# Optimization experiments

Hardware: AMD Instinct MI355X
Metric: run time of the kernel (lower is better)

The kernel has to match this reference:

```python
import jax, jax.numpy as jnp
import numpy as np

N = 50000
E = 800000


def sage_conv(x, edge_index, W_l, b_l, W_r):
    """PyG SAGEConv with mean aggregation.

    out = lin_l(mean_{j in N(i)} x_j) + lin_r(x_i)
    lin_l has bias, lin_r (root weight) has no bias.
    """
    src, dst = edge_index[0], edge_index[1]
    n = x.shape[0]
    msg_sum = jax.ops.segment_sum(x[src], dst, num_segments=n)          # [N, F]
    cnt = jax.ops.segment_sum(jnp.ones((edge_index.shape[1],), x.dtype), dst,
                              num_segments=n)                           # [N]
    mean = msg_sum / jnp.maximum(cnt, 1.0)[:, None]
    return mean @ W_l + b_l + x @ W_r


def setup_inputs() -> dict:
    key = jax.random.key(0)
    ks = jax.random.split(key, 10)
    dims = [(128, 128), (128, 128), (128, 64)]
    inp = {
        "x": jax.random.normal(ks[0], (N, 128), dtype=jnp.float32),
        "edge_index": jax.random.randint(ks[1], (2, E), 0, N, dtype=jnp.int64),
    }
    for i, (fi, fo) in enumerate(dims):
        scale = 1.0 / np.sqrt(fi)
        inp[f"W_l{i}"] = jax.random.uniform(ks[2 + 3 * i - (3 * i) % 1], (fi, fo), jnp.float32, -scale, scale)
        inp[f"b_l{i}"] = jnp.zeros((fo,), jnp.float32)
        inp[f"W_r{i}"] = jax.random.uniform(jax.random.fold_in(ks[3], i), (fi, fo), jnp.float32, -scale, scale)
        inp[f"W_l{i}"] = jax.random.uniform(jax.random.fold_in(ks[2], i), (fi, fo), jnp.float32, -scale, scale)
    return inp


def reference(x, edge_index, W_l0, b_l0, W_r0, W_l1, b_l1, W_r1, W_l2, b_l2, W_r2):
    # Layer 1 + relu (dropout identity in eval mode)
    h = jax.nn.relu(sage_conv(x, edge_index, W_l0, b_l0, W_r0))
    # Layer 2 + relu
    h = jax.nn.relu(sage_conv(h, edge_index, W_l1, b_l1, W_r1))
    # Output layer (no activation)
    return sage_conv(h, edge_index, W_l2, b_l2, W_r2)
```

## Files before the change

### kernel.cpp

```cpp
#include <hip/hip_runtime.h>

static inline int ceil_div(int a, int b) { return (a + b - 1) / b; }

typedef __attribute__((ext_vector_type(8))) short short8;
typedef __attribute__((ext_vector_type(4))) float f32x4;

__device__ __forceinline__ ushort bf16_rne(float v) {
  uint u = __float_as_uint(v);
  return (ushort)((u + 0x7FFFu + ((u >> 16) & 1u)) >> 16);
}


__global__ void k_zero_int(int* __restrict__ p, int n) {
  int i = blockIdx.x * blockDim.x + threadIdx.x;
  if (i < n) p[i] = 0;
}

__global__ void k_count_rank(const int* __restrict__ dst, int* __restrict__ cnt,
                             int* __restrict__ rank, int e) {
  int i0 = (blockIdx.x * blockDim.x + threadIdx.x) * 4;
  if (i0 >= e) return;
  int d[4], r[4];
  if (i0 + 3 < e) {
    int4 dv = *(const int4*)(dst + i0);
    d[0] = dv.x; d[1] = dv.y; d[2] = dv.z; d[3] = dv.w;
  } else {
#pragma unroll
    for (int j = 0; j < 4; ++j) d[j] = (i0 + j < e) ? dst[i0 + j] : 0;
  }
#pragma unroll
  for (int j = 0; j < 4; ++j)
    if (i0 + j < e) r[j] = atomicAdd(&cnt[d[j]], 1);
  if (i0 + 3 < e) {
    *(int4*)(rank + i0) = make_int4(r[0], r[1], r[2], r[3]);
  } else {
#pragma unroll
    for (int j = 0; j < 4; ++j)
      if (i0 + j < e) rank[i0 + j] = r[j];
  }
}

#define SCAN_BS 256
#define SCAN_VPT 4
#define SCAN_CHUNK (SCAN_BS * SCAN_VPT)

__global__ __launch_bounds__(SCAN_BS) void k_blocksum(const int* __restrict__ cnt,
                                                      int* __restrict__ partial, int n) {
  __shared__ int s[SCAN_BS / 64];
  const int tid = threadIdx.x;
  const int base = blockIdx.x * SCAN_CHUNK;
  int sum = 0;
#pragma unroll
  for (int j = 0; j < SCAN_VPT; ++j) {
    int i = base + tid + j * SCAN_BS;
    if (i < n) sum += cnt[i];
  }
#pragma unroll
  for (int off = 32; off > 0; off >>= 1) sum += __shfl_down(sum, off, 64);
  if ((tid & 63) == 0) s[tid >> 6] = sum;
  __syncthreads();
  if (tid == 0) {
    int t = 0;
#pragma unroll
    for (int w = 0; w < SCAN_BS / 64; ++w) t += s[w];
    partial[blockIdx.x] = t;
  }
}

__global__ __launch_bounds__(256) void k_scan_partials(int* __restrict__ partial, int p,
                                                       int* __restrict__ row_ptr, int n_nodes) {
  __shared__ int s[256];
  const int tid = threadIdx.x;
  int carry = 0;
  for (int base = 0; base < p; base += 256) {
    int i = base + tid;
    int v = (i < p) ? partial[i] : 0;
    s[tid] = v;
    __syncthreads();
    for (int off = 1; off < 256; off <<= 1) {
      int t = (tid >= off) ? s[tid - off] : 0;
      __syncthreads();
      s[tid] += t;
      __syncthreads();
    }
    if (i < p) partial[i] = carry + s[tid] - v;
    int tot = s[255];
    __syncthreads();
    carry += tot;
  }
  if (tid == 0) row_ptr[n_nodes] = carry;
}

__global__ __launch_bounds__(SCAN_BS) void k_scatter(const int* __restrict__ cnt,
                                                     const int* __restrict__ partial,
                                                     int* __restrict__ row_ptr,
                                                     float* __restrict__ inv, int n) {
  __shared__ int s[SCAN_BS];
  const int tid = threadIdx.x;
  const int base = blockIdx.x * SCAN_CHUNK;
  const int i0 = base + tid * SCAN_VPT;
  int v[SCAN_VPT];
  int cv[SCAN_VPT];
  int sum = 0;
#pragma unroll
  for (int j = 0; j < SCAN_VPT; ++j) {
    int i = i0 + j;
    int c = (i < n) ? cnt[i] : 0;
    cv[j] = c;
    v[j] = sum;
    sum += c;
  }
  s[tid] = sum;
  __syncthreads();
  for (int off = 1; off < SCAN_BS; off <<= 1) {
    int t = (tid >= off) ? s[tid - off] : 0;
    __syncthreads();
    s[tid] += t;
    __syncthreads();
  }
  const int excl = partial[blockIdx.x] + s[tid] - sum;
#pragma unroll
  for (int j = 0; j < SCAN_VPT; ++j) {
    int i = i0 + j;
    if (i < n) {
      row_ptr[i] = excl + v[j];
      inv[i] = 1.0f / (float)(cv[j] > 1 ? cv[j] : 1);
    }
  }
}

__global__ void k_place(const int* __restrict__ src, const int* __restrict__ dst,
                        const int* __restrict__ rank, const int* __restrict__ row_ptr,
                        ushort* __restrict__ csr16, int e) {
  int i0 = (blockIdx.x * blockDim.x + threadIdx.x) * 4;
  if (i0 >= e) return;
  if (i0 + 3 < e) {
    int4 dv = *(const int4*)(dst + i0);
    int4 sv = *(const int4*)(src + i0);
    int4 rv = *(const int4*)(rank + i0);
    int p0 = row_ptr[dv.x], p1 = row_ptr[dv.y], p2 = row_ptr[dv.z], p3 = row_ptr[dv.w];
    csr16[p0 + rv.x] = (ushort)sv.x;
    csr16[p1 + rv.y] = (ushort)sv.y;
    csr16[p2 + rv.z] = (ushort)sv.z;
    csr16[p3 + rv.w] = (ushort)sv.w;
  } else {
#pragma unroll
    for (int j = 0; j < 4; ++j) {
      int i = i0 + j;
      if (i < e) csr16[row_ptr[dst[i]] + rank[i]] = (ushort)src[i];
    }
  }
}

template <int FOUT>
__global__ void k_pack(const float* __restrict__ Wl, const float* __restrict__ Wr,
                       ushort* __restrict__ hi, ushort* __restrict__ lo) {
  constexpr int NCOL = 2 * FOUT;
  constexpr int NCHUNK = 4 * NCOL * 4;
  int ct = blockIdx.x * 256 + threadIdx.x;
  if (ct >= NCHUNK) return;
  const int g = ct & 3;
  const int nn = (ct >> 2) % NCOL;
  const int kt = ct / (4 * NCOL);
  uint hw[4], lw[4];
#pragma unroll
  for (int w = 0; w < 4; ++w) {
    uint h2[2], l2[2];
#pragma unroll
    for (int t = 0; t < 2; ++t) {
      int j = 2 * w + t;
      int k = kt * 32 + g * 8 + j;
      float v = (nn < FOUT) ? Wl[k * FOUT + nn] : Wr[k * FOUT + (nn - FOUT)];
      uint u = __float_as_uint(v);
      uint h = u >> 16;
      float r = v - __uint_as_float(h << 16);
      uint l = __float_as_uint(r) >> 16;
      h2[t] = h; l2[t] = l;
    }
    hw[w] = h2[0] | (h2[1] << 16);
    lw[w] = l2[0] | (l2[1] << 16);
  }
  ((uint4*)hi)[ct] = make_uint4(hw[0], hw[1], hw[2], hw[3]);
  ((uint4*)lo)[ct] = make_uint4(lw[0], lw[1], lw[2], lw[3]);
}

template <int FOUT>
__global__ __launch_bounds__(256) void k_gemm2(const float* __restrict__ hin,
                                               const ushort* __restrict__ Whi,
                                               const ushort* __restrict__ Wlo,
                                               const float* __restrict__ bias,
                                               ushort* __restrict__ Zb,
                                               float* __restrict__ R, int n) {
  constexpr int NCOL = 2 * FOUT;
  constexpr int NT = NCOL / 64;
  constexpr int MT = 2;
  __shared__ uint4 sA[2][32 * 16];

  const int tid = threadIdx.x;
  const int lane = tid & 63;
  const int wave = tid >> 6;
  const int row0 = blockIdx.x * 32;

  {
    const int srow = tid >> 3;
    const int kc = tid & 7;
    float4 f4[4];
    int g = row0 + srow;
    if (g < n) {
      const float4* hp = (const float4*)(hin + (size_t)g * 128 + kc * 16);
      f4[0] = hp[0]; f4[1] = hp[1]; f4[2] = hp[2]; f4[3] = hp[3];
    } else {
      f4[0] = f4[1] = f4[2] = f4[3] = make_float4(0.f, 0.f, 0.f, 0.f);
    }
    const float* fp = (const float*)f4;
#pragma unroll
    for (int b = 0; b < 2; ++b) {
      uint hw[4], lw[4];
#pragma unroll
      for (int w = 0; w < 4; ++w) {
        float a0 = fp[b * 8 + 2 * w], a1 = fp[b * 8 + 2 * w + 1];
        uint u0 = __float_as_uint(a0), u1 = __float_as_uint(a1);
        uint h0 = u0 >> 16, h1 = u1 >> 16;
        float r0 = a0 - __uint_as_float(h0 << 16);
        float r1 = a1 - __uint_as_float(h1 << 16);
        uint l0 = __float_as_uint(r0) >> 16, l1 = __float_as_uint(r1) >> 16;
        hw[w] = h0 | (h1 << 16);
        lw[w] = l0 | (l1 << 16);
      }
      int slot = (kc * 2 + b) ^ (srow & 7);
      sA[0][srow * 16 + slot] = make_uint4(hw[0], hw[1], hw[2], hw[3]);
      sA[1][srow * 16 + slot] = make_uint4(lw[0], lw[1], lw[2], lw[3]);
    }
  }
  __syncthreads();

  const int n0 = wave * (NCOL / 4);
  const int g16 = lane >> 4;
  const int l16 = lane & 15;

  f32x4 acc[MT][NT];
#pragma unroll
  for (int mt = 0; mt < MT; ++mt)
#pragma unroll
    for (int nt = 0; nt < NT; ++nt) acc[mt][nt] = (f32x4)(0.f);

#pragma unroll
  for (int kt = 0; kt < 4; ++kt) {
    short8 ahi[MT], alo[MT];
#pragma unroll
    for (int mt = 0; mt < MT; ++mt) {
      int row = mt * 16 + l16;
      int slot = (kt * 4 + g16) ^ (row & 7);
      ahi[mt] = *(const short8*)&sA[0][row * 16 + slot];
      alo[mt] = *(const short8*)&sA[1][row * 16 + slot];
    }
    short8 bh[NT];
#pragma unroll
    for (int nt = 0; nt < NT; ++nt) {
      size_t chunk = (size_t)(kt * NCOL + n0 + nt * 16 + l16) * 4 + g16;
      bh[nt] = *(const short8*)(Whi + chunk * 8);
    }
#pragma unroll
    for (int mt = 0; mt < MT; ++mt)
#pragma unroll
      for (int nt = 0; nt < NT; ++nt)
        acc[mt][nt] = __builtin_amdgcn_mfma_f32_16x16x32_bf16(ahi[mt], bh[nt], acc[mt][nt], 0, 0, 0);
#pragma unroll
    for (int mt = 0; mt < MT; ++mt)
#pragma unroll
      for (int nt = 0; nt < NT; ++nt)
        acc[mt][nt] = __builtin_amdgcn_mfma_f32_16x16x32_bf16(alo[mt], bh[nt], acc[mt][nt], 0, 0, 0);
    short8 bl[NT];
#pragma unroll
    for (int nt = 0; nt < NT; ++nt) {
      size_t chunk = (size_t)(kt * NCOL + n0 + nt * 16 + l16) * 4 + g16;
      bl[nt] = *(const short8*)(Wlo + chunk * 8);
    }
#pragma unroll
    for (int mt = 0; mt < MT; ++mt)
#pragma unroll
      for (int nt = 0; nt < NT; ++nt)
        acc[mt][nt] = __builtin_amdgcn_mfma_f32_16x16x32_bf16(ahi[mt], bl[nt], acc[mt][nt], 0, 0, 0);
  }

#pragma unroll
  for (int nt = 0; nt < NT; ++nt) {
    int col = n0 + nt * 16 + l16;
    bool isR = col >= FOUT;
    int cw = isR ? col - FOUT : col;
    float badd = isR ? bias[cw] : 0.f;
#pragma unroll
    for (int mt = 0; mt < MT; ++mt) {
#pragma unroll
      for (int j = 0; j < 4; ++j) {
        int row = row0 + mt * 16 + g16 * 4 + j;
        if (row < n) {
          float v = acc[mt][nt][j] + badd;
          if (isR) R[(size_t)row * FOUT + cw] = v;
          else Zb[(size_t)row * FOUT + cw] = bf16_rne(v);
        }
      }
    }
  }
}

template <int FOUT, bool RELU>
__global__ __launch_bounds__(256) void k_agg2(const ushort* __restrict__ Zb,
                                              const float* __restrict__ R,
                                              const int* __restrict__ row_ptr,
                                              const ushort* __restrict__ csr16,
                                              const float* __restrict__ inv,
                                              float* __restrict__ outp, int n) {
  constexpr int FL = FOUT / 8;
  constexpr int EG = 64 / FL;
  const int lane = threadIdx.x & 63;
  const int node = blockIdx.x * 4 + (threadIdx.x >> 6);
  if (node >= n) return;
  const int c = lane % FL;
  const int eg = lane / FL;

  const int e0 = row_ptr[node];
  const int m = row_ptr[node + 1] - e0;
  const uint4* Z4 = (const uint4*)Zb;

  float acc[8];
#pragma unroll
  for (int k = 0; k < 8; ++k) acc[k] = 0.f;

  int t = eg;
  while (t < m) {
    int ss[4];
#pragma unroll
    for (int j = 0; j < 4; ++j) {
      int tj = t + j * EG;
      int tc = (tj < m) ? tj : (m - 1);
      ss[j] = csr16[e0 + tc];
    }
    uint4 z[4];
#pragma unroll
    for (int j = 0; j < 4; ++j) z[j] = Z4[(size_t)ss[j] * FL + c];
#pragma unroll
    for (int j = 0; j < 4; ++j) {
      if (t + j * EG < m) {
        const uint* zw = (const uint*)&z[j];
#pragma unroll
        for (int w = 0; w < 4; ++w) {
          acc[2 * w]     += __uint_as_float(zw[w] << 16);
          acc[2 * w + 1] += __uint_as_float(zw[w] & 0xFFFF0000u);
        }
      }
    }
    t += 4 * EG;
  }

#pragma unroll
  for (int off = FL; off < 64; off <<= 1) {
#pragma unroll
    for (int k = 0; k < 8; ++k) acc[k] += __shfl_xor(acc[k], off, 64);
  }

  if (eg == 0) {
    const float iv = inv[node];
    const float4* Rp = (const float4*)(R + (size_t)node * FOUT + c * 8);
    float4 r0 = Rp[0], r1 = Rp[1];
    float4 o0, o1;
    o0.x = fmaf(acc[0], iv, r0.x);
    o0.y = fmaf(acc[1], iv, r0.y);
    o0.z = fmaf(acc[2], iv, r0.z);
    o0.w = fmaf(acc[3], iv, r0.w);
    o1.x = fmaf(acc[4], iv, r1.x);
    o1.y = fmaf(acc[5], iv, r1.y);
    o1.z = fmaf(acc[6], iv, r1.z);
    o1.w = fmaf(acc[7], iv, r1.w);
    if (RELU) {
      o0.x = fmaxf(o0.x, 0.f); o0.y = fmaxf(o0.y, 0.f);
      o0.z = fmaxf(o0.z, 0.f); o0.w = fmaxf(o0.w, 0.f);
      o1.x = fmaxf(o1.x, 0.f); o1.y = fmaxf(o1.y, 0.f);
      o1.z = fmaxf(o1.z, 0.f); o1.w = fmaxf(o1.w, 0.f);
    }
    float4* op = (float4*)(outp + (size_t)node * FOUT + c * 8);
    op[0] = o0;
    op[1] = o1;
  }
}


extern "C" void kernel_launch(void* const* d_in, const int* in_sizes, int n_in,
                              void* d_out, int out_size, void* d_ws, size_t ws_size,
                              hipStream_t stream) {
  const float* x   = (const float*)d_in[0];
  const int*   ei  = (const int*)d_in[1];
  const float* Wl0 = (const float*)d_in[2];
  const float* bl0 = (const float*)d_in[3];
  const float* Wr0 = (const float*)d_in[4];
  const float* Wl1 = (const float*)d_in[5];
  const float* bl1 = (const float*)d_in[6];
  const float* Wr1 = (const float*)d_in[7];
  const float* Wl2 = (const float*)d_in[8];
  const float* bl2 = (const float*)d_in[9];
  const float* Wr2 = (const float*)d_in[10];
  float* out = (float*)d_out;

  const int N = in_sizes[0] / 128;
  const int E = in_sizes[1] / 2;
  const int* src = ei;
  const int* dst = ei + E;

  char* w = (char*)d_ws;
  auto alloc = [&](size_t bytes) {
    char* p = w;
    w += (bytes + 255) & ~(size_t)255;
    return p;
  };
  int*    cnt     = (int*)alloc((size_t)N * 4);
  int*    row_ptr = (int*)alloc((size_t)(N + 1) * 4);
  int*    rank    = (int*)alloc((size_t)E * 4);
  ushort* csr16   = (ushort*)alloc((size_t)E * 2 + 256);
  float*  inv     = (float*)alloc((size_t)N * 4);
  int*    partial = (int*)alloc((size_t)ceil_div(N, SCAN_CHUNK) * 4 + 256);
  ushort* Whi0    = (ushort*)alloc((size_t)4 * 256 * 4 * 16);
  ushort* Wlo0    = (ushort*)alloc((size_t)4 * 256 * 4 * 16);
  ushort* Whi1    = (ushort*)alloc((size_t)4 * 256 * 4 * 16);
  ushort* Wlo1    = (ushort*)alloc((size_t)4 * 256 * 4 * 16);
  ushort* Whi2    = (ushort*)alloc((size_t)4 * 128 * 4 * 16);
  ushort* Wlo2    = (ushort*)alloc((size_t)4 * 128 * 4 * 16);
  ushort* BZ      = (ushort*)alloc((size_t)N * 128 * 2);
  float*  BR      = (float*)alloc((size_t)N * 128 * 4);
  float*  B0      = (float*)alloc((size_t)N * 128 * 4);
  (void)ws_size; (void)n_in; (void)out_size;

  const int P = ceil_div(N, SCAN_CHUNK);

  k_pack<128><<<16, 256, 0, stream>>>(Wl0, Wr0, Whi0, Wlo0);
  k_pack<128><<<16, 256, 0, stream>>>(Wl1, Wr1, Whi1, Wlo1);
  k_pack<64><<<8, 256, 0, stream>>>(Wl2, Wr2, Whi2, Wlo2);

  k_zero_int<<<ceil_div(N, 256), 256, 0, stream>>>(cnt, N);
  k_count_rank<<<ceil_div(E, 1024), 256, 0, stream>>>(dst, cnt, rank, E);
  k_blocksum<<<P, SCAN_BS, 0, stream>>>(cnt, partial, N);
  k_scan_partials<<<1, 256, 0, stream>>>(partial, P, row_ptr, N);
  k_scatter<<<P, SCAN_BS, 0, stream>>>(cnt, partial, row_ptr, inv, N);
  k_place<<<ceil_div(E, 1024), 256, 0, stream>>>(src, dst, rank, row_ptr, csr16, E);

  k_gemm2<128><<<ceil_div(N, 32), 256, 0, stream>>>(x, Whi0, Wlo0, bl0, BZ, BR, N);
  k_agg2<128, true><<<ceil_div(N, 4), 256, 0, stream>>>(BZ, BR, row_ptr, csr16, inv, B0, N);

  k_gemm2<128><<<ceil_div(N, 32), 256, 0, stream>>>(B0, Whi1, Wlo1, bl1, BZ, BR, N);
  k_agg2<128, true><<<ceil_div(N, 4), 256, 0, stream>>>(BZ, BR, row_ptr, csr16, inv, B0, N);

  k_gemm2<64><<<ceil_div(N, 32), 256, 0, stream>>>(B0, Whi2, Wlo2, bl2, BZ, BR, N);
  k_agg2<64, false><<<ceil_div(N, 4), 256, 0, stream>>>(BZ, BR, row_ptr, csr16, inv, out, N);
}
```

Measured before the change: 236.9 us.

## Switch GEMMs to single-pass bf16 inputs and store intermediate activations as bf16

Replaces the split hi/lo bf16 emulation of fp32 GEMM (three MFMA passes) with a single bf16 pass, rounding weights and activations to bf16. Inter-layer activations are written by the aggregation kernel as bf16 instead of fp32, and a new conversion kernel casts x to bf16 up front. Edge rank storage shrinks from int to ushort. This cuts MFMA work and activation memory traffic, but loses precision relative to fp32, which may exceed tolerance, and the ushort rank assumes per-node degree below 65536.

```diff
diff --git a/kernel.cpp b/kernel.cpp
--- a/kernel.cpp
+++ b/kernel.cpp
@@ -16,8 +16,21 @@
   if (i < n) p[i] = 0;
 }
 
+__global__ void k_cvt(const float* __restrict__ in, ushort* __restrict__ outp, int n8) {
+  int i = blockIdx.x * blockDim.x + threadIdx.x;
+  if (i >= n8) return;
+  const float4* ip = (const float4*)(in + (size_t)i * 8);
+  float4 a = ip[0], b = ip[1];
+  uint p0 = (uint)bf16_rne(a.x) | ((uint)bf16_rne(a.y) << 16);
+  uint p1 = (uint)bf16_rne(a.z) | ((uint)bf16_rne(a.w) << 16);
+  uint p2 = (uint)bf16_rne(b.x) | ((uint)bf16_rne(b.y) << 16);
+  uint p3 = (uint)bf16_rne(b.z) | ((uint)bf16_rne(b.w) << 16);
+  ((uint4*)outp)[i] = make_uint4(p0, p1, p2, p3);
+}
+
+
 __global__ void k_count_rank(const int* __restrict__ dst, int* __restrict__ cnt,
-                             int* __restrict__ rank, int e) {
+                             ushort* __restrict__ rank, int e) {
   int i0 = (blockIdx.x * blockDim.x + threadIdx.x) * 4;
   if (i0 >= e) return;
   int d[4], r[4];
@@ -32,11 +45,14 @@
   for (int j = 0; j < 4; ++j)
     if (i0 + j < e) r[j] = atomicAdd(&cnt[d[j]], 1);
   if (i0 + 3 < e) {
-    *(int4*)(rank + i0) = make_int4(r[0], r[1], r[2], r[3]);
+    ushort4 rv;
+    rv.x = (ushort)r[0]; rv.y = (ushort)r[1];
+    rv.z = (ushort)r[2]; rv.w = (ushort)r[3];
+    *(ushort4*)(rank + i0) = rv;
   } else {
 #pragma unroll
     for (int j = 0; j < 4; ++j)
-      if (i0 + j < e) rank[i0 + j] = r[j];
+      if (i0 + j < e) rank[i0 + j] = (ushort)r[j];
   }
 }
 
@@ -130,14 +146,14 @@
 }
 
 __global__ void k_place(const int* __restrict__ src, const int* __restrict__ dst,
-                        const int* __restrict__ rank, const int* __restrict__ row_ptr,
+                        const ushort* __restrict__ rank, const int* __restrict__ row_ptr,
                         ushort* __restrict__ csr16, int e) {
   int i0 = (blockIdx.x * blockDim.x + threadIdx.x) * 4;
   if (i0 >= e) return;
   if (i0 + 3 < e) {
     int4 dv = *(const int4*)(dst + i0);
     int4 sv = *(const int4*)(src + i0);
-    int4 rv = *(const int4*)(rank + i0);
+    ushort4 rv = *(const ushort4*)(rank + i0);
     int p0 = row_ptr[dv.x], p1 = row_ptr[dv.y], p2 = row_ptr[dv.z], p3 = row_ptr[dv.w];
     csr16[p0 + rv.x] = (ushort)sv.x;
     csr16[p1 + rv.y] = (ushort)sv.y;
@@ -154,7 +170,7 @@
 
 template <int FOUT>
 __global__ void k_pack(const float* __restrict__ Wl, const float* __restrict__ Wr,
-                       ushort* __restrict__ hi, ushort* __restrict__ lo) {
+                       ushort* __restrict__ hi) {
   constexpr int NCOL = 2 * FOUT;
   constexpr int NCHUNK = 4 * NCOL * 4;
   int ct = blockIdx.x * 256 + threadIdx.x;
@@ -162,75 +178,45 @@
   const int g = ct & 3;
   const int nn = (ct >> 2) % NCOL;
   const int kt = ct / (4 * NCOL);
-  uint hw[4], lw[4];
+  uint hw[4];
 #pragma unroll
   for (int w = 0; w < 4; ++w) {
-    uint h2[2], l2[2];
+    uint h2[2];
 #pragma unroll
     for (int t = 0; t < 2; ++t) {
       int j = 2 * w + t;
       int k = kt * 32 + g * 8 + j;
       float v = (nn < FOUT) ? Wl[k * FOUT + nn] : Wr[k * FOUT + (nn - FOUT)];
-      uint u = __float_as_uint(v);
-      uint h = u >> 16;
-      float r = v - __uint_as_float(h << 16);
-      uint l = __float_as_uint(r) >> 16;
-      h2[t] = h; l2[t] = l;
+      h2[t] = (uint)bf16_rne(v);
     }
     hw[w] = h2[0] | (h2[1] << 16);
-    lw[w] = l2[0] | (l2[1] << 16);
   }
   ((uint4*)hi)[ct] = make_uint4(hw[0], hw[1], hw[2], hw[3]);
-  ((uint4*)lo)[ct] = make_uint4(lw[0], lw[1], lw[2], lw[3]);
 }
 
 template <int FOUT>
-__global__ __launch_bounds__(256) void k_gemm2(const float* __restrict__ hin,
-                                               const ushort* __restrict__ Whi,
-                                               const ushort* __restrict__ Wlo,
-                                               const float* __restrict__ bias,
-                                               ushort* __restrict__ Zb,
-                                               float* __restrict__ R, int n) {
+__global__ __launch_bounds__(256) void k_gemm2b(const ushort* __restrict__ Hb,
+                                                const ushort* __restrict__ Whi,
+                                                const float* __restrict__ bias,
+                                                ushort* __restrict__ Zb,
+                                                float* __restrict__ R, int n) {
   constexpr int NCOL = 2 * FOUT;
   constexpr int NT = NCOL / 64;
   constexpr int MT = 2;
-  __shared__ uint4 sA[2][32 * 16];
+  __shared__ uint4 sA[32 * 16];
 
   const int tid = threadIdx.x;
   const int lane = tid & 63;
   const int wave = tid >> 6;
   const int row0 = blockIdx.x * 32;
 
-  {
-    const int srow = tid >> 3;
-    const int kc = tid & 7;
-    float4 f4[4];
+#pragma unroll
+  for (int c = tid; c < 512; c += 256) {
+    int srow = c >> 4, col16 = c & 15;
     int g = row0 + srow;
-    if (g < n) {
-      const float4* hp = (const float4*)(hin + (size_t)g * 128 + kc * 16);
-      f4[0] = hp[0]; f4[1] = hp[1]; f4[2] = hp[2]; f4[3] = hp[3];
-    } else {
-      f4[0] = f4[1] = f4[2] = f4[3] = make_float4(0.f, 0.f, 0.f, 0.f);
-    }
-    const float* fp = (const float*)f4;
-#pragma unroll
-    for (int b = 0; b < 2; ++b) {
-      uint hw[4], lw[4];
-#pragma unroll
-      for (int w = 0; w < 4; ++w) {
-        float a0 = fp[b * 8 + 2 * w], a1 = fp[b * 8 + 2 * w + 1];
-        uint u0 = __float_as_uint(a0), u1 = __float_as_uint(a1);
-        uint h0 = u0 >> 16, h1 = u1 >> 16;
-        float r0 = a0 - __uint_as_float(h0 << 16);
-        float r1 = a1 - __uint_as_float(h1 << 16);
-        uint l0 = __float_as_uint(r0) >> 16, l1 = __float_as_uint(r1) >> 16;
-        hw[w] = h0 | (h1 << 16);
-        lw[w] = l0 | (l1 << 16);
-      }
-      int slot = (kc * 2 + b) ^ (srow & 7);
-      sA[0][srow * 16 + slot] = make_uint4(hw[0], hw[1], hw[2], hw[3]);
-      sA[1][srow * 16 + slot] = make_uint4(lw[0], lw[1], lw[2], lw[3]);
-    }
+    uint4 v = make_uint4(0u, 0u, 0u, 0u);
+    if (g < n) v = *(const uint4*)(Hb + (size_t)g * 128 + col16 * 8);
+    sA[srow * 16 + (col16 ^ (srow & 7))] = v;
   }
   __syncthreads();
 
@@ -246,13 +232,12 @@
 
 #pragma unroll
   for (int kt = 0; kt < 4; ++kt) {
-    short8 ahi[MT], alo[MT];
+    short8 a[MT];
 #pragma unroll
     for (int mt = 0; mt < MT; ++mt) {
       int row = mt * 16 + l16;
       int slot = (kt * 4 + g16) ^ (row & 7);
-      ahi[mt] = *(const short8*)&sA[0][row * 16 + slot];
-      alo[mt] = *(const short8*)&sA[1][row * 16 + slot];
+      a[mt] = *(const short8*)&sA[row * 16 + slot];
     }
     short8 bh[NT];
 #pragma unroll
@@ -264,23 +249,7 @@
     for (int mt = 0; mt < MT; ++mt)
 #pragma unroll
       for (int nt = 0; nt < NT; ++nt)
-        acc[mt][nt] = __builtin_amdgcn_mfma_f32_16x16x32_bf16(ahi[mt], bh[nt], acc[mt][nt], 0, 0, 0);
-#pragma unroll
-    for (int mt = 0; mt < MT; ++mt)
-#pragma unroll
-      for (int nt = 0; nt < NT; ++nt)
-        acc[mt][nt] = __builtin_amdgcn_mfma_f32_16x16x32_bf16(alo[mt], bh[nt], acc[mt][nt], 0, 0, 0);
-    short8 bl[NT];
-#pragma unroll
-    for (int nt = 0; nt < NT; ++nt) {
-      size_t chunk = (size_t)(kt * NCOL + n0 + nt * 16 + l16) * 4 + g16;
-      bl[nt] = *(const short8*)(Wlo + chunk * 8);
-    }
-#pragma unroll
-    for (int mt = 0; mt < MT; ++mt)
-#pragma unroll
-      for (int nt = 0; nt < NT; ++nt)
-        acc[mt][nt] = __builtin_amdgcn_mfma_f32_16x16x32_bf16(ahi[mt], bl[nt], acc[mt][nt], 0, 0, 0);
+        acc[mt][nt] = __builtin_amdgcn_mfma_f32_16x16x32_bf16(a[mt], bh[nt], acc[mt][nt], 0, 0, 0);
   }
 
 #pragma unroll
@@ -304,13 +273,13 @@
   }
 }
 
-template <int FOUT, bool RELU>
+template <int FOUT, bool RELU, bool OUTB>
 __global__ __launch_bounds__(256) void k_agg2(const ushort* __restrict__ Zb,
                                               const float* __restrict__ R,
                                               const int* __restrict__ row_ptr,
                                               const ushort* __restrict__ csr16,
                                               const float* __restrict__ inv,
-                                              float* __restrict__ outp, int n) {
+                                              void* __restrict__ outp, int n) {
   constexpr int FL = FOUT / 8;
   constexpr int EG = 64 / FL;
   const int lane = threadIdx.x & 63;
@@ -363,24 +332,30 @@
     const float iv = inv[node];
     const float4* Rp = (const float4*)(R + (size_t)node * FOUT + c * 8);
     float4 r0 = Rp[0], r1 = Rp[1];
-    float4 o0, o1;
-    o0.x = fmaf(acc[0], iv, r0.x);
-    o0.y = fmaf(acc[1], iv, r0.y);
-    o0.z = fmaf(acc[2], iv, r0.z);
-    o0.w = fmaf(acc[3], iv, r0.w);
-    o1.x = fmaf(acc[4], iv, r1.x);
-    o1.y = fmaf(acc[5], iv, r1.y);
-    o1.z = fmaf(acc[6], iv, r1.z);
-    o1.w = fmaf(acc[7], iv, r1.w);
+    float o[8];
+    o[0] = fmaf(acc[0], iv, r0.x);
+    o[1] = fmaf(acc[1], iv, r0.y);
+    o[2] = fmaf(acc[2], iv, r0.z);
+    o[3] = fmaf(acc[3], iv, r0.w);
+    o[4] = fmaf(acc[4], iv, r1.x);
+    o[5] = fmaf(acc[5], iv, r1.y);
+    o[6] = fmaf(acc[6], iv, r1.z);
+    o[7] = fmaf(acc[7], iv, r1.w);
     if (RELU) {
-      o0.x = fmaxf(o0.x, 0.f); o0.y = fmaxf(o0.y, 0.f);
-      o0.z = fmaxf(o0.z, 0.f); o0.w = fmaxf(o0.w, 0.f);
-      o1.x = fmaxf(o1.x, 0.f); o1.y = fmaxf(o1.y, 0.f);
-      o1.z = fmaxf(o1.z, 0.f); o1.w = fmaxf(o1.w, 0.f);
-    }
-    float4* op = (float4*)(outp + (size_t)node * FOUT + c * 8);
-    op[0] = o0;
-    op[1] = o1;
+#pragma unroll
+      for (int k = 0; k < 8; ++k) o[k] = fmaxf(o[k], 0.f);
+    }
+    if (OUTB) {
+      uint p[4];
+#pragma unroll
+      for (int w = 0; w < 4; ++w)
+        p[w] = (uint)bf16_rne(o[2 * w]) | ((uint)bf16_rne(o[2 * w + 1]) << 16);
+      ((uint4*)outp)[(size_t)node * FL + c] = make_uint4(p[0], p[1], p[2], p[3]);
+    } else {
+      float4* op = (float4*)((float*)outp + (size_t)node * FOUT + c * 8);
+      op[0] = make_float4(o[0], o[1], o[2], o[3]);
+      op[1] = make_float4(o[4], o[5], o[6], o[7]);
+    }
   }
 }
 
@@ -414,26 +389,25 @@
   };
   int*    cnt     = (int*)alloc((size_t)N * 4);
   int*    row_ptr = (int*)alloc((size_t)(N + 1) * 4);
-  int*    rank    = (int*)alloc((size_t)E * 4);
+  ushort* rank    = (ushort*)alloc((size_t)E * 2 + 256);
   ushort* csr16   = (ushort*)alloc((size_t)E * 2 + 256);
   float*  inv     = (float*)alloc((size_t)N * 4);
   int*    partial = (int*)alloc((size_t)ceil_div(N, SCAN_CHUNK) * 4 + 256);
   ushort* Whi0    = (ushort*)alloc((size_t)4 * 256 * 4 * 16);
-  ushort* Wlo0    = (ushort*)alloc((size_t)4 * 256 * 4 * 16);
   ushort* Whi1    = (ushort*)alloc((size_t)4 * 256 * 4 * 16);
-  ushort* Wlo1    = (ushort*)alloc((size_t)4 * 256 * 4 * 16);
   ushort* Whi2    = (ushort*)alloc((size_t)4 * 128 * 4 * 16);
-  ushort* Wlo2    = (ushort*)alloc((size_t)4 * 128 * 4 * 16);
+  ushort* XB      = (ushort*)alloc((size_t)N * 128 * 2);
   ushort* BZ      = (ushort*)alloc((size_t)N * 128 * 2);
   float*  BR      = (float*)alloc((size_t)N * 128 * 4);
-  float*  B0      = (float*)alloc((size_t)N * 128 * 4);
+  ushort* B0      = (ushort*)alloc((size_t)N * 128 * 2);
   (void)ws_size; (void)n_in; (void)out_size;
 
   const int P = ceil_div(N, SCAN_CHUNK);
 
-  k_pack<128><<<16, 256, 0, stream>>>(Wl0, Wr0, Whi0, Wlo0);
-  k_pack<128><<<16, 256, 0, stream>>>(Wl1, Wr1, Whi1, Wlo1);
-  k_pack<64><<<8, 256, 0, stream>>>(Wl2, Wr2, Whi2, Wlo2);
+  k_pack<128><<<16, 256, 0, stream>>>(Wl0, Wr0, Whi0);
+  k_pack<128><<<16, 256, 0, stream>>>(Wl1, Wr1, Whi1);
+  k_pack<64><<<8, 256, 0, stream>>>(Wl2, Wr2, Whi2);
+  k_cvt<<<ceil_div(N * 16, 256), 256, 0, stream>>>(x, XB, N * 16);
 
   k_zero_int<<<ceil_div(N, 256), 256, 0, stream>>>(cnt, N);
   k_count_rank<<<ceil_div(E, 1024), 256, 0, stream>>>(dst, cnt, rank, E);
@@ -442,12 +416,12 @@
   k_scatter<<<P, SCAN_BS, 0, stream>>>(cnt, partial, row_ptr, inv, N);
   k_place<<<ceil_div(E, 1024), 256, 0, stream>>>(src, dst, rank, row_ptr, csr16, E);
 
-  k_gemm2<128><<<ceil_div(N, 32), 256, 0, stream>>>(x, Whi0, Wlo0, bl0, BZ, BR, N);
-  k_agg2<128, true><<<ceil_div(N, 4), 256, 0, stream>>>(BZ, BR, row_ptr, csr16, inv, B0, N);
-
-  k_gemm2<128><<<ceil_div(N, 32), 256, 0, stream>>>(B0, Whi1, Wlo1, bl1, BZ, BR, N);
-  k_agg2<128, true><<<ceil_div(N, 4), 256, 0, stream>>>(BZ, BR, row_ptr, csr16, inv, B0, N);
-
-  k_gemm2<64><<<ceil_div(N, 32), 256, 0, stream>>>(B0, Whi2, Wlo2, bl2, BZ, BR, N);
-  k_agg2<64, false><<<ceil_div(N, 4), 256, 0, stream>>>(BZ, BR, row_ptr, csr16, inv, out, N);
-}
+  k_gemm2b<128><<<ceil_div(N, 32), 256, 0, stream>>>(XB, Whi0, bl0, BZ, BR, N);
+  k_agg2<128, true, true><<<ceil_div(N, 4), 256, 0, stream>>>(BZ, BR, row_ptr, csr16, inv, B0, N);
+
+  k_gemm2b<128><<<ceil_div(N, 32), 256, 0, stream>>>(B0, Whi1, bl1, BZ, BR, N);
+  k_agg2<128, true, true><<<ceil_div(N, 4), 256, 0, stream>>>(BZ, BR, row_ptr, csr16, inv, B0, N);
+
+  k_gemm2b<64><<<ceil_div(N, 32), 256, 0, stream>>>(B0, Whi2, bl2, BZ, BR, N);
+  k_agg2<64, false, false><<<ceil_div(N, 4), 256, 0, stream>>>(BZ, BR, row_ptr, csr16, inv, out, N);
+}
```

Result: faster. 223.4 us (-5.7%).
